# Performance work log

Measured on AMD Instinct MI355X. Metric: run time of the kernel, lower is better.

The kernel has to match this reference:

```python
import jax, jax.numpy as jnp
import numpy as np

N = 50000      # nodes
E = 640000     # edges
F_IN = 128
F_OUT = 128


def setup_inputs() -> dict:
    key = jax.random.key(0)
    k1, k2, k3, k4, k5 = jax.random.split(key, 5)
    x = jax.random.normal(k1, (N, F_IN), jnp.float32)
    # binary observation mask (torch: mask.float())
    mask = (jax.random.uniform(k2, (N, F_IN)) < 0.5).astype(jnp.float32)
    edge_index = jax.random.randint(k3, (2, E), 0, N, dtype=jnp.int32)
    W = jax.random.normal(k4, (F_OUT, F_IN), jnp.float32) / np.sqrt(F_IN)
    b = jax.random.normal(k5, (F_OUT,), jnp.float32) * 0.01
    return {"x": x, "mask": mask, "edge_index": edge_index, "W": W, "b": b}


def reference(x, mask, edge_index, W, b):
    row, col = edge_index[0], edge_index[1]

    # --- get_symmetrically_normalized_adjacency: DAD = D^-1/2 A D^-1/2 ---
    ones_e = jnp.ones((edge_index.shape[1],), x.dtype)
    deg = jax.ops.segment_sum(ones_e, col, num_segments=N)
    dinv = jnp.where(deg > 0, deg ** -0.5, 0.0)  # inf -> 0
    w = dinv[row] * dinv[col]                    # [E] normalized edge weights

    def spmm(m):  # (adj @ m)[i] = sum_{e: row_e=i} w_e * m[col_e]
        return jax.ops.segment_sum(w[:, None] * m[col], row, num_segments=N)

    # x[x.isnan()] = 0
    x = jnp.nan_to_num(x)

    # adj @ ones_like(x) == rowsum(adj) broadcast over features
    rowsum = jax.ops.segment_sum(w, row, num_segments=N)  # [N]
    numerator = rowsum[:, None] * spmm(mask * x)          # [N, F_IN]
    denominator = spmm(mask)                              # [N, F_IN]
    ratio = jnp.nan_to_num(numerator / denominator)

    return ratio @ W.T + b
```

## Files before the change

### kernel.cpp

```cpp
#include <hip/hip_runtime.h>
#include <math.h>

#define NN 50000
#define NE 640000
#define F  128
#define NB 196
#define ECHUNK 2500
#define WPAD 136

typedef __attribute__((ext_vector_type(8))) short short8;
typedef __attribute__((ext_vector_type(4))) float floatx4;

__device__ inline unsigned f2bf_pk(float f0, float f1) {
    unsigned u0 = __float_as_uint(f0), u1 = __float_as_uint(f1);
    u0 = (u0 + 0x7fffu + ((u0 >> 16) & 1u)) >> 16;
    u1 = (u1 + 0x7fffu + ((u1 >> 16) & 1u)) >> 16;
    return (u1 << 16) | u0;
}

__device__ inline unsigned ilv4(unsigned a, unsigned b) {
    a = (a | (a << 2)) & 0x33u; a = (a | (a << 1)) & 0x55u;
    b = (b | (b << 2)) & 0x33u; b = (b | (b << 1)) & 0x55u;
    return a | (b << 1);
}

__global__ __launch_bounds__(256) void pack_kernel(const float* __restrict__ x,
                                                   const float* __restrict__ mask,
                                                   unsigned* __restrict__ mx,
                                                   unsigned char* __restrict__ bits8) {
    int lane = threadIdx.x & 63;
    int n = blockIdx.x * 4 + (threadIdx.x >> 6);
    float2 xv = ((const float2*)x)[(size_t)n * 64 + lane];
    float2 mv = ((const float2*)mask)[(size_t)n * 64 + lane];
    float x0 = (xv.x != xv.x) ? 0.f : xv.x;
    float x1 = (xv.y != xv.y) ? 0.f : xv.y;
    float p0 = (mv.x != 0.f) ? x0 : 0.f;
    float p1 = (mv.y != 0.f) ? x1 : 0.f;
    mx[(size_t)n * 64 + lane] = f2bf_pk(p0, p1);
    unsigned long long b0 = __ballot(mv.x != 0.f);
    unsigned long long b1 = __ballot(mv.y != 0.f);
    if (lane < 16) {
        unsigned nib0 = (unsigned)(b0 >> (4 * lane)) & 0xFu;
        unsigned nib1 = (unsigned)(b1 >> (4 * lane)) & 0xFu;
        bits8[(size_t)n * 16 + lane] = (unsigned char)ilv4(nib0, nib1);
    }
}

__global__ __launch_bounds__(256) void chist_kernel(const int* __restrict__ row,
                                                    const int* __restrict__ col,
                                                    int* __restrict__ crow,
                                                    int* __restrict__ ccol) {
    __shared__ int hr[NB], hc[NB];
    for (int i = threadIdx.x; i < NB; i += 256) { hr[i] = 0; hc[i] = 0; }
    __syncthreads();
    int e0 = blockIdx.x * ECHUNK, e1 = e0 + ECHUNK;
    for (int e = e0 + threadIdx.x; e < e1; e += 256) {
        atomicAdd(&hr[row[e] >> 8], 1);
        atomicAdd(&hc[col[e] >> 8], 1);
    }
    __syncthreads();
    for (int i = threadIdx.x; i < NB; i += 256) {
        atomicAdd(&crow[i], hr[i]);
        atomicAdd(&ccol[i], hc[i]);
    }
}

__global__ __launch_bounds__(256) void cscan_kernel(const int* __restrict__ crow,
                                                    const int* __restrict__ ccol,
                                                    int* __restrict__ crow_base,
                                                    int* __restrict__ ccol_base,
                                                    int* __restrict__ crow_cur,
                                                    int* __restrict__ ccol_cur,
                                                    int* __restrict__ rowstart) {
    __shared__ int ws[4];
    int t = threadIdx.x, lane = t & 63, wid = t >> 6;
    {
        int v = (t < NB) ? crow[t] : 0;
        int incl = v;
        #pragma unroll
        for (int off = 1; off < 64; off <<= 1) { int s = __shfl_up(incl, off); if (lane >= off) incl += s; }
        if (lane == 63) ws[wid] = incl;
        __syncthreads();
        int wbase = 0;
        for (int k = 0; k < wid; k++) wbase += ws[k];
        int ex = wbase + incl - v;
        if (t < NB) { crow_base[t] = ex; crow_cur[t] = ex; }
        if (t == 0) { crow_base[NB] = NE; rowstart[NN] = NE; }
        __syncthreads();
    }
    {
        int v = (t < NB) ? ccol[t] : 0;
        int incl = v;
        #pragma unroll
        for (int off = 1; off < 64; off <<= 1) { int s = __shfl_up(incl, off); if (lane >= off) incl += s; }
        if (lane == 63) ws[wid] = incl;
        __syncthreads();
        int wbase = 0;
        for (int k = 0; k < wid; k++) wbase += ws[k];
        int ex = wbase + incl - v;
        if (t < NB) { ccol_base[t] = ex; ccol_cur[t] = ex; }
        if (t == 0) ccol_base[NB] = NE;
    }
}

__global__ __launch_bounds__(256) void scatter_kernel(const int* __restrict__ row,
                                                      const int* __restrict__ col,
                                                      int* __restrict__ crow_cur,
                                                      int* __restrict__ ccol_cur,
                                                      unsigned* __restrict__ rrec,
                                                      unsigned char* __restrict__ crec) {
    __shared__ int cntR[NB], cntC[NB], curR[NB], curC[NB];
    for (int i = threadIdx.x; i < NB; i += 256) { cntR[i] = 0; cntC[i] = 0; }
    __syncthreads();
    int e0 = blockIdx.x * ECHUNK, e1 = e0 + ECHUNK;
    for (int e = e0 + threadIdx.x; e < e1; e += 256) {
        atomicAdd(&cntR[row[e] >> 8], 1);
        atomicAdd(&cntC[col[e] >> 8], 1);
    }
    __syncthreads();
    for (int i = threadIdx.x; i < NB; i += 256) {
        curR[i] = atomicAdd(&crow_cur[i], cntR[i]);
        curC[i] = atomicAdd(&ccol_cur[i], cntC[i]);
    }
    __syncthreads();
    for (int e = e0 + threadIdx.x; e < e1; e += 256) {
        int r = row[e], c = col[e];
        int pr = atomicAdd(&curR[r >> 8], 1);
        rrec[pr] = ((unsigned)(r & 255) << 16) | (unsigned)c;
        int pc = atomicAdd(&curC[c >> 8], 1);
        crec[pc] = (unsigned char)(c & 255);
    }
}

__global__ __launch_bounds__(256) void finerow_kernel(const unsigned* __restrict__ rrec,
                                                      const int* __restrict__ crow_base,
                                                      int* __restrict__ rowstart,
                                                      unsigned short* __restrict__ srcs) {
    __shared__ int hist[256];
    __shared__ int ws[4];
    int b = blockIdx.x;
    int s0 = crow_base[b], s1 = crow_base[b + 1];
    int t = threadIdx.x, lane = t & 63, wid = t >> 6;
    hist[t] = 0;
    __syncthreads();
    for (int j = s0 + t; j < s1; j += 256)
        atomicAdd(&hist[(rrec[j] >> 16) & 255], 1);
    __syncthreads();
    int v = hist[t];
    int incl = v;
    #pragma unroll
    for (int off = 1; off < 64; off <<= 1) { int s = __shfl_up(incl, off); if (lane >= off) incl += s; }
    if (lane == 63) ws[wid] = incl;
    __syncthreads();
    int wbase = 0;
    for (int k = 0; k < wid; k++) wbase += ws[k];
    int ex = wbase + incl - v;
    int node = b * 256 + t;
    if (node < NN) rowstart[node] = s0 + ex;
    hist[t] = ex;
    __syncthreads();
    for (int j = s0 + t; j < s1; j += 256) {
        unsigned rec = rrec[j];
        int pos = atomicAdd(&hist[(rec >> 16) & 255], 1);
        srcs[s0 + pos] = (unsigned short)(rec & 0xFFFFu);
    }
}

__global__ __launch_bounds__(256) void finecol_kernel(const unsigned char* __restrict__ crec,
                                                      const int* __restrict__ ccol_base,
                                                      float* __restrict__ dinv) {
    __shared__ int hist[256];
    int b = blockIdx.x;
    int s0 = ccol_base[b], s1 = ccol_base[b + 1];
    int t = threadIdx.x;
    hist[t] = 0;
    __syncthreads();
    for (int j = s0 + t; j < s1; j += 256)
        atomicAdd(&hist[crec[j]], 1);
    __syncthreads();
    int node = b * 256 + t;
    if (node < NN) {
        int d = hist[t];
        dinv[node] = (d > 0) ? rsqrtf((float)d) : 0.0f;
    }
}

__global__ __launch_bounds__(256) void gather_kernel(
        const int* __restrict__ rowstart, const unsigned short* __restrict__ srcs,
        const float* __restrict__ dinv,
        const uint4* __restrict__ mxv, const unsigned char* __restrict__ bits8,
        float* __restrict__ ratio) {
    int lane = threadIdx.x & 63;
    int r = blockIdx.x * 4 + (threadIdx.x >> 6);
    int l16 = lane & 15, sub = lane >> 4;
    int s0 = rowstart[r], s1 = rowstart[r + 1];
    float dr = dinv[r];
    float num[8] = {0.f,0.f,0.f,0.f,0.f,0.f,0.f,0.f};
    float den[8] = {0.f,0.f,0.f,0.f,0.f,0.f,0.f,0.f};
    float S = 0.f;

    for (int j = s0; j < s1; j += 4) {
        int jj = j + sub;
        int cl = (jj < s1) ? jj : (s1 - 1);
        int c = srcs[cl];
        float w = (jj < s1) ? dinv[c] : 0.f;
        uint4 u = mxv[(size_t)c * 16 + l16];
        unsigned mb = bits8[(size_t)c * 16 + l16];
        float f[8];
        f[0] = __uint_as_float(u.x << 16); f[1] = __uint_as_float(u.x & 0xffff0000u);
        f[2] = __uint_as_float(u.y << 16); f[3] = __uint_as_float(u.y & 0xffff0000u);
        f[4] = __uint_as_float(u.z << 16); f[5] = __uint_as_float(u.z & 0xffff0000u);
        f[6] = __uint_as_float(u.w << 16); f[7] = __uint_as_float(u.w & 0xffff0000u);
        S += w;
        #pragma unroll
        for (int q = 0; q < 8; q++) {
            num[q] += w * f[q];
            den[q] += ((mb >> q) & 1u) ? w : 0.f;
        }
    }

    #pragma unroll
    for (int q = 0; q < 8; q++) {
        num[q] += __shfl_xor(num[q], 16); num[q] += __shfl_xor(num[q], 32);
        den[q] += __shfl_xor(den[q], 16); den[q] += __shfl_xor(den[q], 32);
    }
    S += __shfl_xor(S, 16); S += __shfl_xor(S, 32);

    if (sub == 0) {
        float kf = dr * S;
        float o[8];
        #pragma unroll
        for (int q = 0; q < 8; q++)
            o[q] = (den[q] != 0.f) ? kf * num[q] / den[q] : 0.f;
        float4* outp = (float4*)(ratio + (size_t)r * F + l16 * 8);
        outp[0] = make_float4(o[0], o[1], o[2], o[3]);
        outp[1] = make_float4(o[4], o[5], o[6], o[7]);
    }
}

__global__ __launch_bounds__(256) void gemm_kernel(const float* __restrict__ A,
                                                   const float* __restrict__ W,
                                                   const float* __restrict__ bias,
                                                   float* __restrict__ out) {
    __shared__ unsigned short Wlds[F * WPAD];
    int tid = threadIdx.x;

    for (int i = tid * 4; i < F * F; i += 256 * 4) {
        int c = i >> 7, k = i & 127;
        float4 v = *(const float4*)(W + i);
        unsigned lo = f2bf_pk(v.x, v.y);
        unsigned hi = f2bf_pk(v.z, v.w);
        *(uint2*)&Wlds[c * WPAD + k] = make_uint2(lo, hi);
    }
    __syncthreads();

    int lane = tid & 63, wid = tid >> 6;
    int m = lane & 15, quad = lane >> 4;
    int arow = blockIdx.x * 64 + wid * 16 + m;
    int lrow = (arow < NN) ? arow : (NN - 1);
    const float* Arow = A + (size_t)lrow * F + quad * 8;

    floatx4 acc[8];
    #pragma unroll
    for (int nt = 0; nt < 8; nt++) acc[nt] = (floatx4)(0.f);

    #pragma unroll
    for (int step = 0; step < 4; step++) {
        float4 a0 = *(const float4*)(Arow + step * 32);
        float4 a1 = *(const float4*)(Arow + step * 32 + 4);
        union { short8 s; unsigned u[4]; } af;
        af.u[0] = f2bf_pk(a0.x, a0.y);
        af.u[1] = f2bf_pk(a0.z, a0.w);
        af.u[2] = f2bf_pk(a1.x, a1.y);
        af.u[3] = f2bf_pk(a1.z, a1.w);
        #pragma unroll
        for (int nt = 0; nt < 8; nt++) {
            short8 bf = *(const short8*)&Wlds[(nt * 16 + m) * WPAD + step * 32 + quad * 8];
            acc[nt] = __builtin_amdgcn_mfma_f32_16x16x32_bf16(af.s, bf, acc[nt], 0, 0, 0);
        }
    }

    int orow0 = blockIdx.x * 64 + wid * 16 + quad * 4;
    #pragma unroll
    for (int nt = 0; nt < 8; nt++) {
        float bv = bias[nt * 16 + m];
        #pragma unroll
        for (int p = 0; p < 4; p++) {
            int gr = orow0 + p;
            if (gr < NN) out[(size_t)gr * F + nt * 16 + m] = acc[nt][p] + bv;
        }
    }
}

extern "C" void kernel_launch(void* const* d_in, const int* in_sizes, int n_in,
                              void* d_out, int out_size, void* d_ws, size_t ws_size,
                              hipStream_t stream) {
    const float* x    = (const float*)d_in[0];
    const float* mask = (const float*)d_in[1];
    const int*   ei   = (const int*)d_in[2];
    const float* W    = (const float*)d_in[3];
    const float* b    = (const float*)d_in[4];
    float* out = (float*)d_out;

    const int* row = ei;
    const int* col = ei + NE;

    unsigned*       mx        = (unsigned*)d_ws;
    unsigned char*  bits8     = (unsigned char*)(mx + (size_t)NN * 64);
    unsigned short* srcs      = (unsigned short*)(bits8 + (size_t)NN * 16);
    unsigned*       rrec      = (unsigned*)(srcs + NE);
    unsigned char*  crec      = (unsigned char*)(rrec + NE);
    int*            crow      = (int*)(crec + NE);
    int*            ccol      = crow + NB;
    int*            crow_base = ccol + NB;
    int*            ccol_base = crow_base + NB + 1;
    int*            crow_cur  = ccol_base + NB + 1;
    int*            ccol_cur  = crow_cur + NB;
    int*            rowstart  = ccol_cur + NB;
    float*          dinv      = (float*)(rowstart + NN + 1);

    hipMemsetAsync(crow, 0, 2 * NB * sizeof(int), stream);

    pack_kernel<<<NN / 4, 256, 0, stream>>>(x, mask, mx, bits8);
    chist_kernel<<<256, 256, 0, stream>>>(row, col, crow, ccol);
    cscan_kernel<<<1, 256, 0, stream>>>(crow, ccol, crow_base, ccol_base,
                                        crow_cur, ccol_cur, rowstart);
    scatter_kernel<<<256, 256, 0, stream>>>(row, col, crow_cur, ccol_cur, rrec, crec);
    finerow_kernel<<<NB, 256, 0, stream>>>(rrec, crow_base, rowstart, srcs);
    finecol_kernel<<<NB, 256, 0, stream>>>(crec, ccol_base, dinv);
    gather_kernel<<<NN / 4, 256, 0, stream>>>(rowstart, srcs, dinv,
                                              (const uint4*)mx, bits8, out);
    gemm_kernel<<<(NN + 63) / 64, 256, 0, stream>>>(out, W, b, out);
}
```

Before: 212.1 us.

## Merge pack/histogram and fine kernels, co-locate dinv with mask bits, bf16 ratio

Fuses pack and coarse-histogram into one launch, and the row/col fine passes into one launch, cutting kernel count. Per-node mask bits and dinv are packed into a shared 32-byte record so the gather fetches both from one cache line, and the gather loop is unrolled by two. The gather now writes the ratio as bf16 into a workspace buffer, halving that intermediate's traffic and letting the GEMM load bf16 directly instead of converting fp32. Risks include a larger workspace and added register pressure from the unroll.

```diff
diff --git a/kernel.cpp b/kernel.cpp
--- a/kernel.cpp
+++ b/kernel.cpp
@@ -5,6 +5,8 @@
 #define NE 640000
 #define F  128
 #define NB 196
+#define PACKB 12500
+#define CHB 256
 #define ECHUNK 2500
 #define WPAD 136
 
@@ -24,44 +26,46 @@
     return a | (b << 1);
 }
 
-__global__ __launch_bounds__(256) void pack_kernel(const float* __restrict__ x,
-                                                   const float* __restrict__ mask,
-                                                   unsigned* __restrict__ mx,
-                                                   unsigned char* __restrict__ bits8) {
-    int lane = threadIdx.x & 63;
-    int n = blockIdx.x * 4 + (threadIdx.x >> 6);
-    float2 xv = ((const float2*)x)[(size_t)n * 64 + lane];
-    float2 mv = ((const float2*)mask)[(size_t)n * 64 + lane];
-    float x0 = (xv.x != xv.x) ? 0.f : xv.x;
-    float x1 = (xv.y != xv.y) ? 0.f : xv.y;
-    float p0 = (mv.x != 0.f) ? x0 : 0.f;
-    float p1 = (mv.y != 0.f) ? x1 : 0.f;
-    mx[(size_t)n * 64 + lane] = f2bf_pk(p0, p1);
-    unsigned long long b0 = __ballot(mv.x != 0.f);
-    unsigned long long b1 = __ballot(mv.y != 0.f);
-    if (lane < 16) {
-        unsigned nib0 = (unsigned)(b0 >> (4 * lane)) & 0xFu;
-        unsigned nib1 = (unsigned)(b1 >> (4 * lane)) & 0xFu;
-        bits8[(size_t)n * 16 + lane] = (unsigned char)ilv4(nib0, nib1);
-    }
-}
-
-__global__ __launch_bounds__(256) void chist_kernel(const int* __restrict__ row,
-                                                    const int* __restrict__ col,
-                                                    int* __restrict__ crow,
-                                                    int* __restrict__ ccol) {
-    __shared__ int hr[NB], hc[NB];
-    for (int i = threadIdx.x; i < NB; i += 256) { hr[i] = 0; hc[i] = 0; }
-    __syncthreads();
-    int e0 = blockIdx.x * ECHUNK, e1 = e0 + ECHUNK;
-    for (int e = e0 + threadIdx.x; e < e1; e += 256) {
-        atomicAdd(&hr[row[e] >> 8], 1);
-        atomicAdd(&hc[col[e] >> 8], 1);
-    }
-    __syncthreads();
-    for (int i = threadIdx.x; i < NB; i += 256) {
-        atomicAdd(&crow[i], hr[i]);
-        atomicAdd(&ccol[i], hc[i]);
+__global__ __launch_bounds__(256) void pc_kernel(const float* __restrict__ x,
+                                                 const float* __restrict__ mask,
+                                                 const int* __restrict__ row,
+                                                 const int* __restrict__ col,
+                                                 unsigned* __restrict__ mx,
+                                                 unsigned char* __restrict__ rec,
+                                                 int* __restrict__ crow,
+                                                 int* __restrict__ ccol) {
+    if (blockIdx.x < PACKB) {
+        int lane = threadIdx.x & 63;
+        int n = blockIdx.x * 4 + (threadIdx.x >> 6);
+        float2 xv = ((const float2*)x)[(size_t)n * 64 + lane];
+        float2 mv = ((const float2*)mask)[(size_t)n * 64 + lane];
+        float x0 = (xv.x != xv.x) ? 0.f : xv.x;
+        float x1 = (xv.y != xv.y) ? 0.f : xv.y;
+        float p0 = (mv.x != 0.f) ? x0 : 0.f;
+        float p1 = (mv.y != 0.f) ? x1 : 0.f;
+        mx[(size_t)n * 64 + lane] = f2bf_pk(p0, p1);
+        unsigned long long b0 = __ballot(mv.x != 0.f);
+        unsigned long long b1 = __ballot(mv.y != 0.f);
+        if (lane < 16) {
+            unsigned nib0 = (unsigned)(b0 >> (4 * lane)) & 0xFu;
+            unsigned nib1 = (unsigned)(b1 >> (4 * lane)) & 0xFu;
+            rec[(size_t)n * 32 + lane] = (unsigned char)ilv4(nib0, nib1);
+        }
+    } else {
+        __shared__ int hr[NB], hc[NB];
+        for (int i = threadIdx.x; i < NB; i += 256) { hr[i] = 0; hc[i] = 0; }
+        __syncthreads();
+        int bid = blockIdx.x - PACKB;
+        int e0 = bid * ECHUNK, e1 = e0 + ECHUNK;
+        for (int e = e0 + threadIdx.x; e < e1; e += 256) {
+            atomicAdd(&hr[row[e] >> 8], 1);
+            atomicAdd(&hc[col[e] >> 8], 1);
+        }
+        __syncthreads();
+        for (int i = threadIdx.x; i < NB; i += 256) {
+            atomicAdd(&crow[i], hr[i]);
+            atomicAdd(&ccol[i], hc[i]);
+        }
     }
 }
 
@@ -132,90 +136,108 @@
     }
 }
 
-__global__ __launch_bounds__(256) void finerow_kernel(const unsigned* __restrict__ rrec,
-                                                      const int* __restrict__ crow_base,
-                                                      int* __restrict__ rowstart,
-                                                      unsigned short* __restrict__ srcs) {
+__global__ __launch_bounds__(256) void fine_kernel(const unsigned* __restrict__ rrec,
+                                                   const unsigned char* __restrict__ crec,
+                                                   const int* __restrict__ crow_base,
+                                                   const int* __restrict__ ccol_base,
+                                                   int* __restrict__ rowstart,
+                                                   unsigned short* __restrict__ srcs,
+                                                   unsigned char* __restrict__ rec) {
     __shared__ int hist[256];
     __shared__ int ws[4];
-    int b = blockIdx.x;
-    int s0 = crow_base[b], s1 = crow_base[b + 1];
     int t = threadIdx.x, lane = t & 63, wid = t >> 6;
     hist[t] = 0;
     __syncthreads();
-    for (int j = s0 + t; j < s1; j += 256)
-        atomicAdd(&hist[(rrec[j] >> 16) & 255], 1);
-    __syncthreads();
-    int v = hist[t];
-    int incl = v;
-    #pragma unroll
-    for (int off = 1; off < 64; off <<= 1) { int s = __shfl_up(incl, off); if (lane >= off) incl += s; }
-    if (lane == 63) ws[wid] = incl;
-    __syncthreads();
-    int wbase = 0;
-    for (int k = 0; k < wid; k++) wbase += ws[k];
-    int ex = wbase + incl - v;
-    int node = b * 256 + t;
-    if (node < NN) rowstart[node] = s0 + ex;
-    hist[t] = ex;
-    __syncthreads();
-    for (int j = s0 + t; j < s1; j += 256) {
-        unsigned rec = rrec[j];
-        int pos = atomicAdd(&hist[(rec >> 16) & 255], 1);
-        srcs[s0 + pos] = (unsigned short)(rec & 0xFFFFu);
-    }
-}
-
-__global__ __launch_bounds__(256) void finecol_kernel(const unsigned char* __restrict__ crec,
-                                                      const int* __restrict__ ccol_base,
-                                                      float* __restrict__ dinv) {
-    __shared__ int hist[256];
-    int b = blockIdx.x;
-    int s0 = ccol_base[b], s1 = ccol_base[b + 1];
-    int t = threadIdx.x;
-    hist[t] = 0;
-    __syncthreads();
-    for (int j = s0 + t; j < s1; j += 256)
-        atomicAdd(&hist[crec[j]], 1);
-    __syncthreads();
-    int node = b * 256 + t;
-    if (node < NN) {
-        int d = hist[t];
-        dinv[node] = (d > 0) ? rsqrtf((float)d) : 0.0f;
+    if (blockIdx.x < NB) {
+        int b = blockIdx.x;
+        int s0 = crow_base[b], s1 = crow_base[b + 1];
+        for (int j = s0 + t; j < s1; j += 256)
+            atomicAdd(&hist[(rrec[j] >> 16) & 255], 1);
+        __syncthreads();
+        int v = hist[t];
+        int incl = v;
+        #pragma unroll
+        for (int off = 1; off < 64; off <<= 1) { int s = __shfl_up(incl, off); if (lane >= off) incl += s; }
+        if (lane == 63) ws[wid] = incl;
+        __syncthreads();
+        int wbase = 0;
+        for (int k = 0; k < wid; k++) wbase += ws[k];
+        int ex = wbase + incl - v;
+        int node = b * 256 + t;
+        if (node < NN) rowstart[node] = s0 + ex;
+        hist[t] = ex;
+        __syncthreads();
+        for (int j = s0 + t; j < s1; j += 256) {
+            unsigned r2 = rrec[j];
+            int pos = atomicAdd(&hist[(r2 >> 16) & 255], 1);
+            srcs[s0 + pos] = (unsigned short)(r2 & 0xFFFFu);
+        }
+    } else {
+        int b = blockIdx.x - NB;
+        int s0 = ccol_base[b], s1 = ccol_base[b + 1];
+        for (int j = s0 + t; j < s1; j += 256)
+            atomicAdd(&hist[crec[j]], 1);
+        __syncthreads();
+        int node = b * 256 + t;
+        if (node < NN) {
+            int d = hist[t];
+            float dv = (d > 0) ? rsqrtf((float)d) : 0.0f;
+            *(float*)(rec + (size_t)node * 32 + 16) = dv;
+        }
     }
 }
 
 __global__ __launch_bounds__(256) void gather_kernel(
         const int* __restrict__ rowstart, const unsigned short* __restrict__ srcs,
-        const float* __restrict__ dinv,
-        const uint4* __restrict__ mxv, const unsigned char* __restrict__ bits8,
-        float* __restrict__ ratio) {
+        const uint4* __restrict__ mxv, const unsigned char* __restrict__ rec,
+        unsigned* __restrict__ rb) {
     int lane = threadIdx.x & 63;
     int r = blockIdx.x * 4 + (threadIdx.x >> 6);
     int l16 = lane & 15, sub = lane >> 4;
     int s0 = rowstart[r], s1 = rowstart[r + 1];
-    float dr = dinv[r];
+    float dr = *(const float*)(rec + (size_t)r * 32 + 16);
     float num[8] = {0.f,0.f,0.f,0.f,0.f,0.f,0.f,0.f};
     float den[8] = {0.f,0.f,0.f,0.f,0.f,0.f,0.f,0.f};
     float S = 0.f;
 
-    for (int j = s0; j < s1; j += 4) {
-        int jj = j + sub;
-        int cl = (jj < s1) ? jj : (s1 - 1);
-        int c = srcs[cl];
-        float w = (jj < s1) ? dinv[c] : 0.f;
-        uint4 u = mxv[(size_t)c * 16 + l16];
-        unsigned mb = bits8[(size_t)c * 16 + l16];
-        float f[8];
-        f[0] = __uint_as_float(u.x << 16); f[1] = __uint_as_float(u.x & 0xffff0000u);
-        f[2] = __uint_as_float(u.y << 16); f[3] = __uint_as_float(u.y & 0xffff0000u);
-        f[4] = __uint_as_float(u.z << 16); f[5] = __uint_as_float(u.z & 0xffff0000u);
-        f[6] = __uint_as_float(u.w << 16); f[7] = __uint_as_float(u.w & 0xffff0000u);
-        S += w;
-        #pragma unroll
-        for (int q = 0; q < 8; q++) {
-            num[q] += w * f[q];
-            den[q] += ((mb >> q) & 1u) ? w : 0.f;
+    for (int j = s0; j < s1; j += 8) {
+        {
+            int jj = j + sub;
+            int cl = (jj < s1) ? jj : (s1 - 1);
+            int c = srcs[cl];
+            float w = (jj < s1) ? *(const float*)(rec + (size_t)c * 32 + 16) : 0.f;
+            uint4 u = mxv[(size_t)c * 16 + l16];
+            unsigned mb = rec[(size_t)c * 32 + l16];
+            float f[8];
+            f[0] = __uint_as_float(u.x << 16); f[1] = __uint_as_float(u.x & 0xffff0000u);
+            f[2] = __uint_as_float(u.y << 16); f[3] = __uint_as_float(u.y & 0xffff0000u);
+            f[4] = __uint_as_float(u.z << 16); f[5] = __uint_as_float(u.z & 0xffff0000u);
+            f[6] = __uint_as_float(u.w << 16); f[7] = __uint_as_float(u.w & 0xffff0000u);
+            S += w;
+            #pragma unroll
+            for (int q = 0; q < 8; q++) {
+                num[q] += w * f[q];
+                den[q] += ((mb >> q) & 1u) ? w : 0.f;
+            }
+        }
+        {
+            int jj = j + 4 + sub;
+            int cl = (jj < s1) ? jj : (s1 - 1);
+            int c = srcs[cl];
+            float w = (jj < s1) ? *(const float*)(rec + (size_t)c * 32 + 16) : 0.f;
+            uint4 u = mxv[(size_t)c * 16 + l16];
+            unsigned mb = rec[(size_t)c * 32 + l16];
+            float f[8];
+            f[0] = __uint_as_float(u.x << 16); f[1] = __uint_as_float(u.x & 0xffff0000u);
+            f[2] = __uint_as_float(u.y << 16); f[3] = __uint_as_float(u.y & 0xffff0000u);
+            f[4] = __uint_as_float(u.z << 16); f[5] = __uint_as_float(u.z & 0xffff0000u);
+            f[6] = __uint_as_float(u.w << 16); f[7] = __uint_as_float(u.w & 0xffff0000u);
+            S += w;
+            #pragma unroll
+            for (int q = 0; q < 8; q++) {
+                num[q] += w * f[q];
+                den[q] += ((mb >> q) & 1u) ? w : 0.f;
+            }
         }
     }
 
@@ -232,13 +254,16 @@
         #pragma unroll
         for (int q = 0; q < 8; q++)
             o[q] = (den[q] != 0.f) ? kf * num[q] / den[q] : 0.f;
-        float4* outp = (float4*)(ratio + (size_t)r * F + l16 * 8);
-        outp[0] = make_float4(o[0], o[1], o[2], o[3]);
-        outp[1] = make_float4(o[4], o[5], o[6], o[7]);
-    }
-}
-
-__global__ __launch_bounds__(256) void gemm_kernel(const float* __restrict__ A,
+        uint4 pk;
+        pk.x = f2bf_pk(o[0], o[1]);
+        pk.y = f2bf_pk(o[2], o[3]);
+        pk.z = f2bf_pk(o[4], o[5]);
+        pk.w = f2bf_pk(o[6], o[7]);
+        ((uint4*)rb)[(size_t)r * 16 + l16] = pk;
+    }
+}
+
+__global__ __launch_bounds__(256) void gemm_kernel(const unsigned short* __restrict__ Ab,
                                                    const float* __restrict__ W,
                                                    const float* __restrict__ bias,
                                                    float* __restrict__ out) {
@@ -258,7 +283,7 @@
     int m = lane & 15, quad = lane >> 4;
     int arow = blockIdx.x * 64 + wid * 16 + m;
     int lrow = (arow < NN) ? arow : (NN - 1);
-    const float* Arow = A + (size_t)lrow * F + quad * 8;
+    const unsigned short* Arow = Ab + (size_t)lrow * F + quad * 8;
 
     floatx4 acc[8];
     #pragma unroll
@@ -266,17 +291,11 @@
 
     #pragma unroll
     for (int step = 0; step < 4; step++) {
-        float4 a0 = *(const float4*)(Arow + step * 32);
-        float4 a1 = *(const float4*)(Arow + step * 32 + 4);
-        union { short8 s; unsigned u[4]; } af;
-        af.u[0] = f2bf_pk(a0.x, a0.y);
-        af.u[1] = f2bf_pk(a0.z, a0.w);
-        af.u[2] = f2bf_pk(a1.x, a1.y);
-        af.u[3] = f2bf_pk(a1.z, a1.w);
+        short8 af = *(const short8*)(Arow + step * 32);
         #pragma unroll
         for (int nt = 0; nt < 8; nt++) {
             short8 bf = *(const short8*)&Wlds[(nt * 16 + m) * WPAD + step * 32 + quad * 8];
-            acc[nt] = __builtin_amdgcn_mfma_f32_16x16x32_bf16(af.s, bf, acc[nt], 0, 0, 0);
+            acc[nt] = __builtin_amdgcn_mfma_f32_16x16x32_bf16(af, bf, acc[nt], 0, 0, 0);
         }
     }
 
@@ -306,10 +325,11 @@
     const int* col = ei + NE;
 
     unsigned*       mx        = (unsigned*)d_ws;
-    unsigned char*  bits8     = (unsigned char*)(mx + (size_t)NN * 64);
-    unsigned short* srcs      = (unsigned short*)(bits8 + (size_t)NN * 16);
-    unsigned*       rrec      = (unsigned*)(srcs + NE);
-    unsigned char*  crec      = (unsigned char*)(rrec + NE);
+    unsigned*       rb        = mx + (size_t)NN * 64;
+    unsigned char*  rec       = (unsigned char*)(rb + (size_t)NN * 64);
+    unsigned*       rrec      = (unsigned*)(rec + (size_t)NN * 32);
+    unsigned short* srcs      = (unsigned short*)(rrec + NE);
+    unsigned char*  crec      = (unsigned char*)(srcs + NE);
     int*            crow      = (int*)(crec + NE);
     int*            ccol      = crow + NB;
     int*            crow_base = ccol + NB;
@@ -317,18 +337,16 @@
     int*            crow_cur  = ccol_base + NB + 1;
     int*            ccol_cur  = crow_cur + NB;
     int*            rowstart  = ccol_cur + NB;
-    float*          dinv      = (float*)(rowstart + NN + 1);
 
     hipMemsetAsync(crow, 0, 2 * NB * sizeof(int), stream);
 
-    pack_kernel<<<NN / 4, 256, 0, stream>>>(x, mask, mx, bits8);
-    chist_kernel<<<256, 256, 0, stream>>>(row, col, crow, ccol);
+    pc_kernel<<<PACKB + CHB, 256, 0, stream>>>(x, mask, row, col, mx, rec, crow, ccol);
     cscan_kernel<<<1, 256, 0, stream>>>(crow, ccol, crow_base, ccol_base,
                                         crow_cur, ccol_cur, rowstart);
-    scatter_kernel<<<256, 256, 0, stream>>>(row, col, crow_cur, ccol_cur, rrec, crec);
-    finerow_kernel<<<NB, 256, 0, stream>>>(rrec, crow_base, rowstart, srcs);
-    finecol_kernel<<<NB, 256, 0, stream>>>(crec, ccol_base, dinv);
-    gather_kernel<<<NN / 4, 256, 0, stream>>>(rowstart, srcs, dinv,
-                                              (const uint4*)mx, bits8, out);
-    gemm_kernel<<<(NN + 63) / 64, 256, 0, stream>>>(out, W, b, out);
-}
+    scatter_kernel<<<CHB, 256, 0, stream>>>(row, col, crow_cur, ccol_cur, rrec, crec);
+    fine_kernel<<<2 * NB, 256, 0, stream>>>(rrec, crec, crow_base, ccol_base,
+                                            rowstart, srcs, rec);
+    gather_kernel<<<NN / 4, 256, 0, stream>>>(rowstart, srcs,
+                                              (const uint4*)mx, rec, rb);
+    gemm_kernel<<<(NN + 63) / 64, 256, 0, stream>>>((const unsigned short*)rb, W, b, out);
+}
```

Result: faster. 197.1 us (-7.1%).
